# Kernel tuning notes

Measured on AMD Instinct MI355X. Metric: run time of the kernel, lower is better.

## Reference

```python
import jax, jax.numpy as jnp
import numpy as np

B, T, H, V = 32, 256, 1024, 256


def setup_inputs() -> dict:
    key = jax.random.key(0)
    ks = jax.random.split(key, 12)
    xavier = float(np.sqrt(6.0 / (H + V)))
    inp = {
        "x": jax.random.randint(ks[0], (B, T), 0, V, dtype=jnp.int64),
        "targets": jax.random.randint(ks[1], (B, T), 0, V, dtype=jnp.int64),
        "h0": jnp.zeros((B, H), jnp.float32),
        "c0": jnp.zeros((B, H), jnp.float32),
        "h1": jnp.zeros((B, H), jnp.float32),
        "c1": jnp.zeros((B, H), jnp.float32),
        # learned params
        "emb": jax.random.normal(ks[2], (V, H), jnp.float32) * 0.05,
        "W_ih0": jax.random.normal(ks[3], (H, 4 * H), jnp.float32) / np.sqrt(H),
        "W_hh0": jax.random.normal(ks[4], (H, 4 * H), jnp.float32) / np.sqrt(H),
        "b0": jnp.zeros((4 * H,), jnp.float32),
        "W_ih1": jax.random.normal(ks[5], (H, 4 * H), jnp.float32) / np.sqrt(H),
        "W_hh1": jax.random.normal(ks[6], (H, 4 * H), jnp.float32) / np.sqrt(H),
        "b1": jnp.zeros((4 * H,), jnp.float32),
        "W_out": jax.random.uniform(ks[7], (H, V), jnp.float32, -xavier, xavier),
        "b_out": jnp.zeros((V,), jnp.float32),
    }
    return inp


def _lstm_cell(h, c, inp, W_ih, W_hh, b):
    # gates: [B, 4H] -> i, f, g, o
    z = inp @ W_ih + h @ W_hh + b
    i, f, g, o = jnp.split(z, 4, axis=-1)
    c_new = jax.nn.sigmoid(f) * c + jax.nn.sigmoid(i) * jnp.tanh(g)
    h_new = jax.nn.sigmoid(o) * jnp.tanh(c_new)
    return h_new, c_new


def reference(x, targets, h0, c0, h1, c1, emb, W_ih0, W_hh0, b0,
              W_ih1, W_hh1, b1, W_out, b_out):
    # Teacher-forcing branch: embed targets, feed embedding at every step.
    embeddings = emb[targets]            # [B, T, H]
    e_seq = jnp.swapaxes(embeddings, 0, 1)  # [T, B, H] for scan over time

    def step(carry, e_t):
        (h0, c0), (h1, c1) = carry
        h0, c0 = _lstm_cell(h0, c0, e_t, W_ih0, W_hh0, b0)
        h1, c1 = _lstm_cell(h1, c1, h0, W_ih1, W_hh1, b1)
        logit = h1 @ W_out + b_out       # [B, V]
        return ((h0, c0), (h1, c1)), logit

    carry0 = ((h0, c0), (h1, c1))
    carry_f, logits_tbv = jax.lax.scan(step, carry0, e_seq)
    logits = jnp.swapaxes(logits_tbv, 0, 1)  # [B, T, V]
    (h0f, c0f), (h1f, c1f) = carry_f
    return logits, h0f, c0f, h1f, c1f
```

## Files before the change

kernel.cpp:

```cpp
#include <hip/hip_runtime.h>
#include <cstdint>


typedef float    f32x4 __attribute__((ext_vector_type(4)));
typedef short    s16x8 __attribute__((ext_vector_type(8)));
typedef unsigned u32x4 __attribute__((ext_vector_type(4)));

#define DEV __device__ __forceinline__

DEV unsigned short f2bf(float x){
  unsigned u = __builtin_bit_cast(unsigned, x);
  unsigned r = (u + 0x7fffu + ((u >> 16) & 1u)) >> 16;
  return (unsigned short)r;
}
DEV float bf2f(unsigned short b){ return __builtin_bit_cast(float, ((unsigned)b) << 16); }

DEV s16x8 ld16(const void* p){ return *(const s16x8*)p; }

DEV f32x4 MF(s16x8 a, s16x8 b, f32x4 c){
  return __builtin_amdgcn_mfma_f32_16x16x32_bf16(a, b, c, 0, 0, 0);
}

#define LDC(dst, ptr)  asm volatile("global_load_dwordx4 %0, %1, off sc0 sc1" : "=v"(dst) : "v"(ptr))
#define LDP(dst, ptr)  asm volatile("global_load_dwordx4 %0, %1, off"         : "=v"(dst) : "v"(ptr))
#define WAITVM(n) do { asm volatile("s_waitcnt vmcnt(" #n ")" ::: "memory"); \
                       __builtin_amdgcn_sched_barrier(0); } while (0)
#define CFENCE()  asm volatile("" ::: "memory")
#define TRIPLE(Cmn, Ahm, Alm, Bhn, Bln) do { \
    Cmn = MF(Ahm, Bhn, Cmn); Cmn = MF(Ahm, Bln, Cmn); Cmn = MF(Alm, Bhn, Cmn); } while (0)

DEV void st16c(void* p, u32x4 v){
  asm volatile("global_store_dwordx4 %0, %1, off sc0 sc1" :: "v"(p), "v"(v) : "memory");
}
DEV void set_flag(int* p, int v){
  __hip_atomic_store(p, v, __ATOMIC_RELAXED, __HIP_MEMORY_SCOPE_AGENT);
}
template<int SLP>
DEV void pollT(const int* f, int lane, int target){
  const int* p0 = f + lane * 8;
  const int* p1 = f + (64 + lane) * 8;
  for (;;) {
    int a = __hip_atomic_load(p0, __ATOMIC_RELAXED, __HIP_MEMORY_SCOPE_AGENT);
    int b = __hip_atomic_load(p1, __ATOMIC_RELAXED, __HIP_MEMORY_SCOPE_AGENT);
    if (__all((a >= target) && (b >= target))) break;
    __builtin_amdgcn_s_sleep(SLP);
  }
  CFENCE();
}
DEV char* h0slot(char* wa0, char* s0, char* hi, int s){
  return (s == 0) ? s0 : ((s <= 128) ? wa0 + ((size_t)(s - 1) << 17)
                                     : hi  + ((size_t)(s - 129) << 17));
}

DEV void halfgemm8(const char* smemMat, const char* ALb, const char* Bb,
                   int wgl, int ksb, int lane, f32x4 (&C)[2][2]) {
  s16x8 P[3][4], AL[3][2];
  #pragma unroll
  for (int d = 0; d < 2; ++d) {
    #pragma unroll
    for (int q = 0; q < 4; ++q) LDP(P[d][q], Bb + ((q * 32 + ksb + d) << 10) + lane * 16);
    LDP(AL[d][0], ALb + ((((wgl * 2 + 0) * 2 + 1) * 32 + ksb + d) << 10) + lane * 16);
    LDP(AL[d][1], ALb + ((((wgl * 2 + 1) * 2 + 1) * 32 + ksb + d) << 10) + lane * 16);
  }
  #pragma unroll
  for (int i = 0; i < 8; ++i) {
    const int ks = ksb + i;
    if (i < 6) {
      #pragma unroll
      for (int q = 0; q < 4; ++q) LDP(P[(i + 2) % 3][q], Bb + ((q * 32 + ks + 2) << 10) + lane * 16);
      LDP(AL[(i + 2) % 3][0], ALb + ((((wgl * 2 + 0) * 2 + 1) * 32 + ks + 2) << 10) + lane * 16);
      LDP(AL[(i + 2) % 3][1], ALb + ((((wgl * 2 + 1) * 2 + 1) * 32 + ks + 2) << 10) + lane * 16);
    }
    s16x8 Ah0 = ld16(smemMat + ((0 * 32 + ks) << 10) + lane * 16);
    s16x8 Ah1 = ld16(smemMat + ((1 * 32 + ks) << 10) + lane * 16);
    if (i < 6) { WAITVM(12); } else if (i == 6) { WAITVM(6); } else { WAITVM(0); }
    TRIPLE(C[0][0], Ah0, AL[i % 3][0], P[i % 3][0], P[i % 3][2]);
    TRIPLE(C[0][1], Ah0, AL[i % 3][0], P[i % 3][1], P[i % 3][3]);
    TRIPLE(C[1][0], Ah1, AL[i % 3][1], P[i % 3][0], P[i % 3][2]);
    TRIPLE(C[1][1], Ah1, AL[i % 3][1], P[i % 3][1], P[i % 3][3]);
  }
}

__global__ void prep_wfrag(const float* __restrict__ W0, const float* __restrict__ W1,
                           const float* __restrict__ W2, const float* __restrict__ W3,
                           char* D0, char* D1, char* D2, char* D3) {
  int gid = blockIdx.x * 256 + threadIdx.x;
  int lane = gid & 63, ks = (gid >> 6) & 31, jb = (gid >> 11) & 255, mat = gid >> 19;
  const float* S = (mat == 0) ? W0 : (mat == 1) ? W1 : (mat == 2) ? W2 : W3;
  char* D = (mat == 0) ? D0 : (mat == 1) ? D1 : (mat == 2) ? D2 : D3;
  int jp = jb * 16 + (lane & 15), u = jp >> 2, g = jp & 3;
  int kb = ks * 32 + (lane >> 4) * 8;
  s16x8 vh, vl;
  #pragma unroll
  for (int i = 0; i < 8; ++i) {
    float x = S[(kb + i) * 4096 + g * 1024 + u];
    unsigned short h = f2bf(x);
    vh[i] = (short)h;
    vl[i] = (short)f2bf(x - bf2f(h));
  }
  *(s16x8*)(D + (((jb * 2 + 0) * 32 + ks) << 10) + lane * 16) = vh;
  *(s16x8*)(D + (((jb * 2 + 1) * 32 + ks) << 10) + lane * 16) = vl;
}

__global__ void prep_bfrag(const float* __restrict__ emb, const float* __restrict__ Wout,
                           char* Demb, char* Dwout) {
  int gid = blockIdx.x * 256 + threadIdx.x;
  int lane = gid & 63, ks = (gid >> 6) & 31, vb = (gid >> 11) & 15, which = gid >> 15;
  int v = vb * 16 + (lane & 15), kb = ks * 32 + (lane >> 4) * 8;
  s16x8 vh, vl;
  #pragma unroll
  for (int i = 0; i < 8; ++i) {
    float x = which ? Wout[(kb + i) * 256 + v] : emb[v * 1024 + kb + i];
    unsigned short h = f2bf(x);
    vh[i] = (short)h;
    vl[i] = (short)f2bf(x - bf2f(h));
  }
  char* D = which ? Dwout : Demb;
  *(s16x8*)(D + (((vb * 2 + 0) * 32 + ks) << 10) + lane * 16) = vh;
  *(s16x8*)(D + (((vb * 2 + 1) * 32 + ks) << 10) + lane * 16) = vl;
}

__global__ void prep_hinit(const float* __restrict__ h0, const float* __restrict__ h1,
                           char* h0s0, char* h1f) {
  int gid = blockIdx.x * 256 + threadIdx.x;
  int lane = gid & 63, ks = (gid >> 6) & 31, nt = (gid >> 11) & 1, which = gid >> 12;
  const float* S = which ? h1 : h0;
  char* D = which ? h1f : h0s0;
  int b = nt * 16 + (lane & 15), kb = ks * 32 + (lane >> 4) * 8;
  s16x8 vh, vl;
  #pragma unroll
  for (int i = 0; i < 8; ++i) {
    float x = S[b * 1024 + kb + i];
    unsigned short h = f2bf(x);
    vh[i] = (short)h;
    vl[i] = (short)f2bf(x - bf2f(h));
  }
  *(s16x8*)(D + (((0 * 2 + nt) * 32 + ks) << 10) + lane * 16) = vh;
  *(s16x8*)(D + (((1 * 2 + nt) * 32 + ks) << 10) + lane * 16) = vl;
}

__global__ void prep_misc(const float* __restrict__ b1, float* b1i, int* f0a, int* f1a) {
  int i = blockIdx.x * 256 + threadIdx.x;
  if (i < 4096) b1i[i] = b1[(i & 3) * 1024 + (i >> 2)];
  if (i < 1024) { f0a[i] = -1; f1a[i] = -1; }
}

__global__ __launch_bounds__(256, 1) void lstm_persist(
    const int* __restrict__ tgt,
    const float* __restrict__ c0_in, const float* __restrict__ c1_in,
    const float* __restrict__ b0, const float* __restrict__ b_out,
    char* __restrict__ WA0, const char* __restrict__ WA1, const char* __restrict__ WA2,
    const char* __restrict__ WAi0, const char* __restrict__ WoutB, const char* __restrict__ embB,
    float* __restrict__ E0, const float* __restrict__ b1i,
    char* __restrict__ h0s0, char* __restrict__ h0hi, char* __restrict__ h1frag,
    int* __restrict__ f0, int* __restrict__ f1,
    float* __restrict__ out)
{
  extern __shared__ char smem[];
  constexpr int PART = 131072;
  constexpr int RP   = 131072 + 16384;
  const int tid = threadIdx.x, lane = tid & 63, wv = tid >> 6;
  const int wg = blockIdx.x;
  const bool isL0 = (wg < 128);
  const int wgl = isL0 ? wg : (wg - 128);
  const int l15 = lane & 15, l4 = lane >> 4;
  const int mi_e = wv >> 1, nt_e = wv & 1;

  __builtin_amdgcn_fence(__ATOMIC_ACQUIRE, "agent");

  if (isL0) {
    u32x4 tmp[8];
    for (int blk = 0; blk < 4; ++blk) {
      #pragma unroll
      for (int q = 0; q < 8; ++q) {
        int idx = tid + (blk * 8 + q) * 256;
        int l16 = idx & 63, ks = (idx >> 6) & 31, mi = (idx >> 11) & 1, part = idx >> 12;
        LDC(tmp[q], WA0 + ((((wgl * 2 + mi) * 2 + part) * 32 + ks) << 10) + l16 * 16);
      }
      WAITVM(0);
      #pragma unroll
      for (int q = 0; q < 8; ++q) {
        int idx = tid + (blk * 8 + q) * 256;
        int l16 = idx & 63, ks = (idx >> 6) & 31, mi = (idx >> 11) & 1, part = idx >> 12;
        *(u32x4*)(smem + (((part * 2 + mi) * 32 + ks) << 10) + l16 * 16) = tmp[q];
      }
    }
  } else {
    for (int idx = tid; idx < 8192; idx += 256) {
      int l16 = idx & 63, ks = (idx >> 6) & 31, mi = (idx >> 11) & 1, mat = idx >> 12;
      const char* W = mat ? WA2 : WA1;
      u32x4 v = *(const u32x4*)(W + ((((wgl * 2 + mi) * 2 + 0) * 32 + ks) << 10) + l16 * 16);
      *(u32x4*)(smem + (((mat * 2 + mi) * 32 + ks) << 10) + l16 * 16) = v;
    }
  }

  if (isL0) {
    f32x4 C[2][4];
    #pragma unroll
    for (int a = 0; a < 2; ++a)
      #pragma unroll
      for (int b = 0; b < 4; ++b) C[a][b] = 0.0f;
    for (int ks = 0; ks < 32; ++ks) {
      s16x8 Ah0, Ah1, Al0, Al1;
      LDC(Ah0, WAi0 + ((((wgl * 2 + 0) * 2 + 0) * 32 + ks) << 10) + lane * 16);
      LDC(Ah1, WAi0 + ((((wgl * 2 + 1) * 2 + 0) * 32 + ks) << 10) + lane * 16);
      LDC(Al0, WAi0 + ((((wgl * 2 + 0) * 2 + 1) * 32 + ks) << 10) + lane * 16);
      LDC(Al1, WAi0 + ((((wgl * 2 + 1) * 2 + 1) * 32 + ks) << 10) + lane * 16);
      WAITVM(0);
      #pragma unroll
      for (int v4 = 0; v4 < 4; ++v4) {
        int vb = wv * 4 + v4;
        s16x8 Bh = ld16(embB + (((vb * 2 + 0) * 32 + ks) << 10) + lane * 16);
        s16x8 Bl = ld16(embB + (((vb * 2 + 1) * 32 + ks) << 10) + lane * 16);
        TRIPLE(C[0][v4], Ah0, Al0, Bh, Bl);
        TRIPLE(C[1][v4], Ah1, Al1, Bh, Bl);
      }
    }
    #pragma unroll
    for (int mi = 0; mi < 2; ++mi) {
      int jb4 = wgl * 32 + mi * 16 + l4 * 4;
      int u = jb4 >> 2;
      f32x4 bb;
      #pragma unroll
      for (int r = 0; r < 4; ++r) bb[r] = b0[r * 1024 + u];
      #pragma unroll
      for (int v4 = 0; v4 < 4; ++v4) {
        int v = (wv * 4 + v4) * 16 + l15;
        *(f32x4*)(E0 + v * 4096 + jb4) = C[mi][v4] + bb;
      }
    }
  }

  float cst;
  {
    const float* cs = isL0 ? c0_in : c1_in;
    cst = cs[(nt_e * 16 + l15) * 1024 + wgl * 8 + mi_e * 4 + l4];
  }
  f32x4 b1z = {0.f, 0.f, 0.f, 0.f};
  if (!isL0) b1z = *(const f32x4*)(b1i + wgl * 32 + mi_e * 16 + (l4 << 2));

  __syncthreads();
  if (tid == 0) set_flag((isL0 ? f0 : f1) + wgl * 8, 0);

  if (isL0) {
    for (int t = 0; t < 256; ++t) {
      const int s = t + 1;
      f32x4 C[2][2];
      #pragma unroll
      for (int a = 0; a < 2; ++a)
        #pragma unroll
        for (int b = 0; b < 2; ++b) C[a][b] = 0.0f;

      int tv = tgt[(nt_e * 16 + l15) * 256 + t];
      f32x4 e0v = *(const f32x4*)(E0 + (size_t)tv * 4096 + wgl * 32 + mi_e * 16 + (l4 << 2));
      pollT<1>(f0, lane, t);
      const char* Bb = h0slot(WA0, h0s0, h0hi, t);
      const int ksb = wv * 8;
      s16x8 P[3][4];
      #pragma unroll
      for (int d = 0; d < 2; ++d)
        #pragma unroll
        for (int q = 0; q < 4; ++q) LDP(P[d][q], Bb + ((q * 32 + ksb + d) << 10) + lane * 16);
      #pragma unroll
      for (int i = 0; i < 8; ++i) {
        const int ks = ksb + i;
        if (i < 6) {
          #pragma unroll
          for (int q = 0; q < 4; ++q) LDP(P[(i + 2) % 3][q], Bb + ((q * 32 + ks + 2) << 10) + lane * 16);
        }
        s16x8 Ah0 = ld16(smem + ((0 * 32 + ks) << 10) + lane * 16);
        s16x8 Ah1 = ld16(smem + ((1 * 32 + ks) << 10) + lane * 16);
        s16x8 Al0 = ld16(smem + ((2 * 32 + ks) << 10) + lane * 16);
        s16x8 Al1 = ld16(smem + ((3 * 32 + ks) << 10) + lane * 16);
        if (i < 6) { WAITVM(8); } else if (i == 6) { WAITVM(4); } else { WAITVM(0); }
        TRIPLE(C[0][0], Ah0, Al0, P[i % 3][0], P[i % 3][2]);
        TRIPLE(C[0][1], Ah0, Al0, P[i % 3][1], P[i % 3][3]);
        TRIPLE(C[1][0], Ah1, Al1, P[i % 3][0], P[i % 3][2]);
        TRIPLE(C[1][1], Ah1, Al1, P[i % 3][1], P[i % 3][3]);
      }

      #pragma unroll
      for (int mi = 0; mi < 2; ++mi)
        #pragma unroll
        for (int nt = 0; nt < 2; ++nt)
          *(f32x4*)(smem + PART + ((wv * 4 + mi * 2 + nt) << 10) + lane * 16) = C[mi][nt];
      __syncthreads();

      {
        f32x4 z = *(const f32x4*)(smem + PART + ((0 * 4 + wv) << 10) + lane * 16);
        #pragma unroll
        for (int w = 1; w < 4; ++w)
          z += *(const f32x4*)(smem + PART + ((w * 4 + wv) << 10) + lane * 16);
        z += e0v;
        float ig = 1.f / (1.f + __expf(-z[0]));
        float fg = 1.f / (1.f + __expf(-z[1]));
        float og = 1.f / (1.f + __expf(-z[3]));
        float cn = fg * cst + ig * tanhf(z[2]);
        float hn = og * tanhf(cn);
        cst = cn;
        unsigned short hb = f2bf(hn);
        unsigned short lb = f2bf(hn - bf2f(hb));
        *(short*)(smem + RP + ((0 + nt_e) * 16 + l15) * 16 + (mi_e * 4 + l4) * 2) = (short)hb;
        *(short*)(smem + RP + ((2 + nt_e) * 16 + l15) * 16 + (mi_e * 4 + l4) * 2) = (short)lb;
        if (t == 255) {
          int u = wgl * 8 + mi_e * 4 + l4, b = nt_e * 16 + l15;
          out[2097152 + b * 1024 + u] = hn;
          out[2097152 + 32768 + b * 1024 + u] = cn;
        }
      }
      __syncthreads();

      if (wv == 0) {
        char* hd = h0slot(WA0, h0s0, h0hi, s);
        u32x4 v = *(const u32x4*)(smem + RP + lane * 16);
        char* dst = hd + (((lane >> 4) * 32 + (wgl >> 2)) << 10) + ((wgl & 3) * 16 + l15) * 16;
        st16c(dst, v);
        asm volatile("s_waitcnt vmcnt(0)" ::: "memory");
        if (lane == 0) set_flag(f0 + wgl * 8, s);
      }
    }
  } else {
    f32x4 zpre;
    {
      pollT<2>(f0, lane, 1);
      f32x4 C2[2][2];
      #pragma unroll
      for (int a = 0; a < 2; ++a)
        #pragma unroll
        for (int b = 0; b < 2; ++b) C2[a][b] = 0.0f;
      halfgemm8(smem, WA1, h0slot(WA0, h0s0, h0hi, 1), wgl, wv * 8, lane, C2);
      #pragma unroll
      for (int mi = 0; mi < 2; ++mi)
        #pragma unroll
        for (int nt = 0; nt < 2; ++nt)
          *(f32x4*)(smem + PART + ((wv * 4 + mi * 2 + nt) << 10) + lane * 16) = C2[mi][nt];
      __syncthreads();
      zpre = *(const f32x4*)(smem + PART + ((0 * 4 + wv) << 10) + lane * 16);
      #pragma unroll
      for (int w = 1; w < 4; ++w)
        zpre += *(const f32x4*)(smem + PART + ((w * 4 + wv) << 10) + lane * 16);
      __syncthreads();
    }

    for (int t = 0; t < 256; ++t) {
      const int s = t + 1;
      f32x4 C[2][2];
      #pragma unroll
      for (int a = 0; a < 2; ++a)
        #pragma unroll
        for (int b = 0; b < 2; ++b) C[a][b] = 0.0f;

      pollT<1>(f1, lane, t);
      halfgemm8(smem + 65536, WA2, h1frag + (size_t)t * 131072, wgl, wv * 8, lane, C);

      #pragma unroll
      for (int mi = 0; mi < 2; ++mi)
        #pragma unroll
        for (int nt = 0; nt < 2; ++nt)
          *(f32x4*)(smem + PART + ((wv * 4 + mi * 2 + nt) << 10) + lane * 16) = C[mi][nt];
      __syncthreads();

      {
        f32x4 z = *(const f32x4*)(smem + PART + ((0 * 4 + wv) << 10) + lane * 16);
        #pragma unroll
        for (int w = 1; w < 4; ++w)
          z += *(const f32x4*)(smem + PART + ((w * 4 + wv) << 10) + lane * 16);
        z += zpre + b1z;
        float ig = 1.f / (1.f + __expf(-z[0]));
        float fg = 1.f / (1.f + __expf(-z[1]));
        float og = 1.f / (1.f + __expf(-z[3]));
        float cn = fg * cst + ig * tanhf(z[2]);
        float hn = og * tanhf(cn);
        cst = cn;
        unsigned short hb = f2bf(hn);
        unsigned short lb = f2bf(hn - bf2f(hb));
        *(short*)(smem + RP + ((0 + nt_e) * 16 + l15) * 16 + (mi_e * 4 + l4) * 2) = (short)hb;
        *(short*)(smem + RP + ((2 + nt_e) * 16 + l15) * 16 + (mi_e * 4 + l4) * 2) = (short)lb;
        if (t == 255) {
          int u = wgl * 8 + mi_e * 4 + l4, b = nt_e * 16 + l15;
          out[2097152 + 65536 + b * 1024 + u] = hn;
          out[2097152 + 65536 + 32768 + b * 1024 + u] = cn;
        }
      }
      __syncthreads();

      if (wv == 0) {
        char* hd = h1frag + (size_t)s * 131072;
        u32x4 v = *(const u32x4*)(smem + RP + lane * 16);
        char* dst = hd + (((lane >> 4) * 32 + (wgl >> 2)) << 10) + ((wgl & 3) * 16 + l15) * 16;
        st16c(dst, v);
        asm volatile("s_waitcnt vmcnt(0)" ::: "memory");
        if (lane == 0) set_flag(f1 + wgl * 8, s);
      }

      if (t < 255) {
        pollT<2>(f0, lane, t + 2);
        f32x4 C2[2][2];
        #pragma unroll
        for (int a = 0; a < 2; ++a)
          #pragma unroll
          for (int b = 0; b < 2; ++b) C2[a][b] = 0.0f;
        halfgemm8(smem, WA1, h0slot(WA0, h0s0, h0hi, t + 2), wgl, wv * 8, lane, C2);
        #pragma unroll
        for (int mi = 0; mi < 2; ++mi)
          #pragma unroll
          for (int nt = 0; nt < 2; ++nt)
            *(f32x4*)(smem + PART + ((wv * 4 + mi * 2 + nt) << 10) + lane * 16) = C2[mi][nt];
        __syncthreads();
        zpre = *(const f32x4*)(smem + PART + ((0 * 4 + wv) << 10) + lane * 16);
        #pragma unroll
        for (int w = 1; w < 4; ++w)
          zpre += *(const f32x4*)(smem + PART + ((w * 4 + wv) << 10) + lane * 16);
        __syncthreads();
      }
    }
  }

  {
    const int tp = isL0 ? wgl : (128 + wgl);
    pollT<32>(f1, lane, tp + 1);
    const char* A = h1frag + (size_t)(tp + 1) * 131072;
    f32x4 C[2][4];
    #pragma unroll
    for (int a = 0; a < 2; ++a)
      #pragma unroll
      for (int b = 0; b < 4; ++b) C[a][b] = 0.0f;
    s16x8 QA[4], QB[4];
    #pragma unroll
    for (int q = 0; q < 4; ++q) LDP(QA[q], A + ((q * 32 + 0) << 10) + lane * 16);
    for (int kk = 0; kk < 16; ++kk) {
      const int ks = kk * 2;
      #pragma unroll
      for (int q = 0; q < 4; ++q) LDP(QB[q], A + ((q * 32 + ks + 1) << 10) + lane * 16);
      asm volatile("s_waitcnt vmcnt(4)" ::: "memory");
      __builtin_amdgcn_sched_barrier(0);
      #pragma unroll
      for (int v4 = 0; v4 < 4; ++v4) {
        int vb = wv * 4 + v4;
        s16x8 Bh = ld16(WoutB + (((vb * 2 + 0) * 32 + ks) << 10) + lane * 16);
        s16x8 Bl = ld16(WoutB + (((vb * 2 + 1) * 32 + ks) << 10) + lane * 16);
        C[0][v4] = MF(QA[0], Bh, C[0][v4]); C[0][v4] = MF(QA[0], Bl, C[0][v4]); C[0][v4] = MF(QA[2], Bh, C[0][v4]);
        C[1][v4] = MF(QA[1], Bh, C[1][v4]); C[1][v4] = MF(QA[1], Bl, C[1][v4]); C[1][v4] = MF(QA[3], Bh, C[1][v4]);
      }
      if (kk < 15) {
        #pragma unroll
        for (int q = 0; q < 4; ++q) LDP(QA[q], A + ((q * 32 + ks + 2) << 10) + lane * 16);
        asm volatile("s_waitcnt vmcnt(4)" ::: "memory");
      } else {
        asm volatile("s_waitcnt vmcnt(0)" ::: "memory");
      }
      __builtin_amdgcn_sched_barrier(0);
      #pragma unroll
      for (int v4 = 0; v4 < 4; ++v4) {
        int vb = wv * 4 + v4;
        s16x8 Bh = ld16(WoutB + (((vb * 2 + 0) * 32 + ks + 1) << 10) + lane * 16);
        s16x8 Bl = ld16(WoutB + (((vb * 2 + 1) * 32 + ks + 1) << 10) + lane * 16);
        C[0][v4] = MF(QB[0], Bh, C[0][v4]); C[0][v4] = MF(QB[0], Bl, C[0][v4]); C[0][v4] = MF(QB[2], Bh, C[0][v4]);
        C[1][v4] = MF(QB[1], Bh, C[1][v4]); C[1][v4] = MF(QB[1], Bl, C[1][v4]); C[1][v4] = MF(QB[3], Bh, C[1][v4]);
      }
    }
    #pragma unroll
    for (int nt = 0; nt < 2; ++nt)
      #pragma unroll
      for (int v4 = 0; v4 < 4; ++v4) {
        int v = (wv * 4 + v4) * 16 + l15;
        float bo = b_out[v];
        #pragma unroll
        for (int r = 0; r < 4; ++r) {
          int b = nt * 16 + l4 * 4 + r;
          out[((size_t)b * 256 + tp) * 256 + v] = C[nt][v4][r] + bo;
        }
      }
  }
}

extern "C" void kernel_launch(void* const* d_in, const int* in_sizes, int n_in,
                              void* d_out, int out_size, void* d_ws, size_t ws_size,
                              hipStream_t stream) {
  const int*   targets = (const int*)d_in[1];
  const float* h0_in   = (const float*)d_in[2];
  const float* c0_in   = (const float*)d_in[3];
  const float* h1_in   = (const float*)d_in[4];
  const float* c1_in   = (const float*)d_in[5];
  const float* emb     = (const float*)d_in[6];
  const float* W_ih0   = (const float*)d_in[7];
  const float* W_hh0   = (const float*)d_in[8];
  const float* b0      = (const float*)d_in[9];
  const float* W_ih1   = (const float*)d_in[10];
  const float* W_hh1   = (const float*)d_in[11];
  const float* b1      = (const float*)d_in[12];
  const float* W_out   = (const float*)d_in[13];
  const float* b_out   = (const float*)d_in[14];
  float* out = (float*)d_out;

  char* ws = (char*)d_ws;
  char*  WA0    = ws;
  char*  WA1    = ws + 16777216;
  char*  WA2    = ws + 33554432;
  char*  WoutB  = ws + 50331648;
  char*  embB   = ws + 51380224;
  float* E0     = (float*)(ws + 52428800);
  float* b1i    = (float*)(ws + 56623104);
  int*   f0     = (int*)(ws + 56639488);
  int*   f1     = (int*)(ws + 56643584);
  char*  h0s0   = ws + 56647680;
  char*  h0hi   = ws + 56778752;
  char*  h1frag = ws + 73555968;
  char*  WAi0   = h1frag + 16777216;

  prep_misc <<<18,   256, 0, stream>>>(b1, b1i, f0, f1);
  prep_wfrag<<<8192, 256, 0, stream>>>(W_hh0, W_ih1, W_hh1, W_ih0, WA0, WA1, WA2, WAi0);
  prep_bfrag<<<256,  256, 0, stream>>>(emb, W_out, embB, WoutB);
  prep_hinit<<<32,   256, 0, stream>>>(h0_in, h1_in, h0s0, h1frag);

  hipFuncSetAttribute(reinterpret_cast<const void*>(lstm_persist),
                      hipFuncAttributeMaxDynamicSharedMemorySize, 148480);
  lstm_persist<<<256, 256, 148480, stream>>>(
      targets, c0_in, c1_in, b0, b_out,
      WA0, WA1, WA2, WAi0, WoutB, embB,
      E0, b1i, h0s0, h0hi, h1frag, f0, f1, out);
}
```

Baseline: 1.729 ms.

## Split layer-1 waves between recurrent and input GEMMs and pack flags

In layer-1 workgroups, two waves now compute the recurrent W_hh1·h1 half-GEMM over 16 k-steps while the other two compute the next step's W_ih1·h0 input projection. The input projection is double-buffered in shared memory, which removes the serial second GEMM phase and its two extra barriers from each timestep. Progress flags are also packed contiguously instead of spaced 8 ints apart, so each poll touches fewer cache lines. The recurrent critical path now runs on half the waves with longer k-loops, and shared memory use grows.

```diff
diff --git a/kernel.cpp b/kernel.cpp
--- a/kernel.cpp
+++ b/kernel.cpp
@@ -36,9 +36,9 @@
   __hip_atomic_store(p, v, __ATOMIC_RELAXED, __HIP_MEMORY_SCOPE_AGENT);
 }
 template<int SLP>
-DEV void pollT(const int* f, int lane, int target){
-  const int* p0 = f + lane * 8;
-  const int* p1 = f + (64 + lane) * 8;
+DEV void pollP(const int* f, int lane, int target){
+  const int* p0 = f + lane;
+  const int* p1 = f + 64 + lane;
   for (;;) {
     int a = __hip_atomic_load(p0, __ATOMIC_RELAXED, __HIP_MEMORY_SCOPE_AGENT);
     int b = __hip_atomic_load(p1, __ATOMIC_RELAXED, __HIP_MEMORY_SCOPE_AGENT);
@@ -52,7 +52,8 @@
                                      : hi  + ((size_t)(s - 129) << 17));
 }
 
-DEV void halfgemm8(const char* smemMat, const char* ALb, const char* Bb,
+template<int ITERS>
+DEV void halfgemmT(const char* smemMat, const char* ALb, const char* Bb,
                    int wgl, int ksb, int lane, f32x4 (&C)[2][2]) {
   s16x8 P[3][4], AL[3][2];
   #pragma unroll
@@ -63,9 +64,9 @@
     LDP(AL[d][1], ALb + ((((wgl * 2 + 1) * 2 + 1) * 32 + ksb + d) << 10) + lane * 16);
   }
   #pragma unroll
-  for (int i = 0; i < 8; ++i) {
+  for (int i = 0; i < ITERS; ++i) {
     const int ks = ksb + i;
-    if (i < 6) {
+    if (i < ITERS - 2) {
       #pragma unroll
       for (int q = 0; q < 4; ++q) LDP(P[(i + 2) % 3][q], Bb + ((q * 32 + ks + 2) << 10) + lane * 16);
       LDP(AL[(i + 2) % 3][0], ALb + ((((wgl * 2 + 0) * 2 + 1) * 32 + ks + 2) << 10) + lane * 16);
@@ -73,7 +74,7 @@
     }
     s16x8 Ah0 = ld16(smemMat + ((0 * 32 + ks) << 10) + lane * 16);
     s16x8 Ah1 = ld16(smemMat + ((1 * 32 + ks) << 10) + lane * 16);
-    if (i < 6) { WAITVM(12); } else if (i == 6) { WAITVM(6); } else { WAITVM(0); }
+    if (i < ITERS - 2) { WAITVM(12); } else if (i == ITERS - 2) { WAITVM(6); } else { WAITVM(0); }
     TRIPLE(C[0][0], Ah0, AL[i % 3][0], P[i % 3][0], P[i % 3][2]);
     TRIPLE(C[0][1], Ah0, AL[i % 3][0], P[i % 3][1], P[i % 3][3]);
     TRIPLE(C[1][0], Ah1, AL[i % 3][1], P[i % 3][0], P[i % 3][2]);
@@ -157,8 +158,11 @@
     float* __restrict__ out)
 {
   extern __shared__ char smem[];
-  constexpr int PART = 131072;
-  constexpr int RP   = 131072 + 16384;
+  constexpr int PART  = 131072;
+  constexpr int RP0   = 131072 + 16384;
+  constexpr int PARTc = 131072;
+  constexpr int ZPRE  = 131072 + 8192;
+  constexpr int RP1   = 131072 + 24576;
   const int tid = threadIdx.x, lane = tid & 63, wv = tid >> 6;
   const int wg = blockIdx.x;
   const bool isL0 = (wg < 128);
@@ -240,7 +244,7 @@
   if (!isL0) b1z = *(const f32x4*)(b1i + wgl * 32 + mi_e * 16 + (l4 << 2));
 
   __syncthreads();
-  if (tid == 0) set_flag((isL0 ? f0 : f1) + wgl * 8, 0);
+  if (tid == 0) set_flag((isL0 ? f0 : f1) + wgl, 0);
 
   if (isL0) {
     for (int t = 0; t < 256; ++t) {
@@ -253,7 +257,7 @@
 
       int tv = tgt[(nt_e * 16 + l15) * 256 + t];
       f32x4 e0v = *(const f32x4*)(E0 + (size_t)tv * 4096 + wgl * 32 + mi_e * 16 + (l4 << 2));
-      pollT<1>(f0, lane, t);
+      pollP<1>(f0, lane, t);
       const char* Bb = h0slot(WA0, h0s0, h0hi, t);
       const int ksb = wv * 8;
       s16x8 P[3][4];
@@ -300,8 +304,8 @@
         cst = cn;
         unsigned short hb = f2bf(hn);
         unsigned short lb = f2bf(hn - bf2f(hb));
-        *(short*)(smem + RP + ((0 + nt_e) * 16 + l15) * 16 + (mi_e * 4 + l4) * 2) = (short)hb;
-        *(short*)(smem + RP + ((2 + nt_e) * 16 + l15) * 16 + (mi_e * 4 + l4) * 2) = (short)lb;
+        *(short*)(smem + RP0 + ((0 + nt_e) * 16 + l15) * 16 + (mi_e * 4 + l4) * 2) = (short)hb;
+        *(short*)(smem + RP0 + ((2 + nt_e) * 16 + l15) * 16 + (mi_e * 4 + l4) * 2) = (short)lb;
         if (t == 255) {
           int u = wgl * 8 + mi_e * 4 + l4, b = nt_e * 16 + l15;
           out[2097152 + b * 1024 + u] = hn;
@@ -312,60 +316,69 @@
 
       if (wv == 0) {
         char* hd = h0slot(WA0, h0s0, h0hi, s);
-        u32x4 v = *(const u32x4*)(smem + RP + lane * 16);
+        u32x4 v = *(const u32x4*)(smem + RP0 + lane * 16);
         char* dst = hd + (((lane >> 4) * 32 + (wgl >> 2)) << 10) + ((wgl & 3) * 16 + l15) * 16;
         st16c(dst, v);
         asm volatile("s_waitcnt vmcnt(0)" ::: "memory");
-        if (lane == 0) set_flag(f0 + wgl * 8, s);
+        if (lane == 0) set_flag(f0 + wgl, s);
       }
     }
   } else {
-    f32x4 zpre;
-    {
-      pollT<2>(f0, lane, 1);
-      f32x4 C2[2][2];
+    pollP<2>(f0, lane, 1);
+    if (wv >= 2) {
+      f32x4 C[2][2];
       #pragma unroll
       for (int a = 0; a < 2; ++a)
         #pragma unroll
-        for (int b = 0; b < 2; ++b) C2[a][b] = 0.0f;
-      halfgemm8(smem, WA1, h0slot(WA0, h0s0, h0hi, 1), wgl, wv * 8, lane, C2);
+        for (int b = 0; b < 2; ++b) C[a][b] = 0.0f;
+      halfgemmT<16>(smem, WA1, h0slot(WA0, h0s0, h0hi, 1), wgl, (wv - 2) * 16, lane, C);
       #pragma unroll
       for (int mi = 0; mi < 2; ++mi)
         #pragma unroll
         for (int nt = 0; nt < 2; ++nt)
-          *(f32x4*)(smem + PART + ((wv * 4 + mi * 2 + nt) << 10) + lane * 16) = C2[mi][nt];
-      __syncthreads();
-      zpre = *(const f32x4*)(smem + PART + ((0 * 4 + wv) << 10) + lane * 16);
-      #pragma unroll
-      for (int w = 1; w < 4; ++w)
-        zpre += *(const f32x4*)(smem + PART + ((w * 4 + wv) << 10) + lane * 16);
-      __syncthreads();
+          *(f32x4*)(smem + ZPRE + ((0 * 8 + (wv - 2) * 4 + mi * 2 + nt) << 10) + lane * 16) = C[mi][nt];
     }
 
     for (int t = 0; t < 256; ++t) {
       const int s = t + 1;
-      f32x4 C[2][2];
-      #pragma unroll
-      for (int a = 0; a < 2; ++a)
-        #pragma unroll
-        for (int b = 0; b < 2; ++b) C[a][b] = 0.0f;
-
-      pollT<1>(f1, lane, t);
-      halfgemm8(smem + 65536, WA2, h1frag + (size_t)t * 131072, wgl, wv * 8, lane, C);
-
-      #pragma unroll
-      for (int mi = 0; mi < 2; ++mi)
-        #pragma unroll
-        for (int nt = 0; nt < 2; ++nt)
-          *(f32x4*)(smem + PART + ((wv * 4 + mi * 2 + nt) << 10) + lane * 16) = C[mi][nt];
+      const int cur = t & 1;
+      pollP<1>(f1, lane, t);
+      if (t < 255) pollP<2>(f0, lane, t + 2);
+
+      if (wv < 2) {
+        f32x4 C[2][2];
+        #pragma unroll
+        for (int a = 0; a < 2; ++a)
+          #pragma unroll
+          for (int b = 0; b < 2; ++b) C[a][b] = 0.0f;
+        halfgemmT<16>(smem + 65536, WA2, h1frag + (size_t)t * 131072, wgl, wv * 16, lane, C);
+        #pragma unroll
+        for (int mi = 0; mi < 2; ++mi)
+          #pragma unroll
+          for (int nt = 0; nt < 2; ++nt)
+            *(f32x4*)(smem + PARTc + ((wv * 4 + mi * 2 + nt) << 10) + lane * 16) = C[mi][nt];
+      } else {
+        f32x4 C[2][2];
+        #pragma unroll
+        for (int a = 0; a < 2; ++a)
+          #pragma unroll
+          for (int b = 0; b < 2; ++b) C[a][b] = 0.0f;
+        const int sl = (t < 255) ? (t + 2) : 256;
+        halfgemmT<16>(smem, WA1, h0slot(WA0, h0s0, h0hi, sl), wgl, (wv - 2) * 16, lane, C);
+        #pragma unroll
+        for (int mi = 0; mi < 2; ++mi)
+          #pragma unroll
+          for (int nt = 0; nt < 2; ++nt)
+            *(f32x4*)(smem + ZPRE + (((cur ^ 1) * 8 + (wv - 2) * 4 + mi * 2 + nt) << 10) + lane * 16) = C[mi][nt];
+      }
       __syncthreads();
 
       {
-        f32x4 z = *(const f32x4*)(smem + PART + ((0 * 4 + wv) << 10) + lane * 16);
-        #pragma unroll
-        for (int w = 1; w < 4; ++w)
-          z += *(const f32x4*)(smem + PART + ((w * 4 + wv) << 10) + lane * 16);
-        z += zpre + b1z;
+        f32x4 z = *(const f32x4*)(smem + PARTc + ((0 * 4 + wv) << 10) + lane * 16);
+        z += *(const f32x4*)(smem + PARTc + ((1 * 4 + wv) << 10) + lane * 16);
+        z += *(const f32x4*)(smem + ZPRE + ((cur * 8 + 0 * 4 + wv) << 10) + lane * 16);
+        z += *(const f32x4*)(smem + ZPRE + ((cur * 8 + 1 * 4 + wv) << 10) + lane * 16);
+        z += b1z;
         float ig = 1.f / (1.f + __expf(-z[0]));
         float fg = 1.f / (1.f + __expf(-z[1]));
         float og = 1.f / (1.f + __expf(-z[3]));
@@ -374,8 +387,8 @@
         cst = cn;
         unsigned short hb = f2bf(hn);
         unsigned short lb = f2bf(hn - bf2f(hb));
-        *(short*)(smem + RP + ((0 + nt_e) * 16 + l15) * 16 + (mi_e * 4 + l4) * 2) = (short)hb;
-        *(short*)(smem + RP + ((2 + nt_e) * 16 + l15) * 16 + (mi_e * 4 + l4) * 2) = (short)lb;
+        *(short*)(smem + RP1 + ((0 + nt_e) * 16 + l15) * 16 + (mi_e * 4 + l4) * 2) = (short)hb;
+        *(short*)(smem + RP1 + ((2 + nt_e) * 16 + l15) * 16 + (mi_e * 4 + l4) * 2) = (short)lb;
         if (t == 255) {
           int u = wgl * 8 + mi_e * 4 + l4, b = nt_e * 16 + l15;
           out[2097152 + 65536 + b * 1024 + u] = hn;
@@ -386,39 +399,18 @@
 
       if (wv == 0) {
         char* hd = h1frag + (size_t)s * 131072;
-        u32x4 v = *(const u32x4*)(smem + RP + lane * 16);
+        u32x4 v = *(const u32x4*)(smem + RP1 + lane * 16);
         char* dst = hd + (((lane >> 4) * 32 + (wgl >> 2)) << 10) + ((wgl & 3) * 16 + l15) * 16;
         st16c(dst, v);
         asm volatile("s_waitcnt vmcnt(0)" ::: "memory");
-        if (lane == 0) set_flag(f1 + wgl * 8, s);
-      }
-
-      if (t < 255) {
-        pollT<2>(f0, lane, t + 2);
-        f32x4 C2[2][2];
-        #pragma unroll
-        for (int a = 0; a < 2; ++a)
-          #pragma unroll
-          for (int b = 0; b < 2; ++b) C2[a][b] = 0.0f;
-        halfgemm8(smem, WA1, h0slot(WA0, h0s0, h0hi, t + 2), wgl, wv * 8, lane, C2);
-        #pragma unroll
-        for (int mi = 0; mi < 2; ++mi)
-          #pragma unroll
-          for (int nt = 0; nt < 2; ++nt)
-            *(f32x4*)(smem + PART + ((wv * 4 + mi * 2 + nt) << 10) + lane * 16) = C2[mi][nt];
-        __syncthreads();
-        zpre = *(const f32x4*)(smem + PART + ((0 * 4 + wv) << 10) + lane * 16);
-        #pragma unroll
-        for (int w = 1; w < 4; ++w)
-          zpre += *(const f32x4*)(smem + PART + ((w * 4 + wv) << 10) + lane * 16);
-        __syncthreads();
+        if (lane == 0) set_flag(f1 + wgl, s);
       }
     }
   }
 
   {
     const int tp = isL0 ? wgl : (128 + wgl);
-    pollT<32>(f1, lane, tp + 1);
+    pollP<32>(f1, lane, tp + 1);
     const char* A = h1frag + (size_t)(tp + 1) * 131072;
     f32x4 C[2][4];
     #pragma unroll
@@ -514,8 +506,8 @@
   prep_hinit<<<32,   256, 0, stream>>>(h0_in, h1_in, h0s0, h1frag);
 
   hipFuncSetAttribute(reinterpret_cast<const void*>(lstm_persist),
-                      hipFuncAttributeMaxDynamicSharedMemorySize, 148480);
-  lstm_persist<<<256, 256, 148480, stream>>>(
+                      hipFuncAttributeMaxDynamicSharedMemorySize, 156672);
+  lstm_persist<<<256, 256, 156672, stream>>>(
       targets, c0_in, c1_in, b0, b_out,
       WA0, WA1, WA2, WAi0, WoutB, embB,
       E0, b1i, h0s0, h0hi, h1frag, f0, f1, out);
```

Result: slower. 3.233 ms (+87.0%).

## Issue all K-slab loads up front and pack sync flags contiguously

Applied to the files above, without the earlier changes.

Replaces the 3-deep rotating prefetch in the recurrent GEMMs with issuing all eight K-step loads at once, then draining them with descending vmcnt waits. This puts more memory requests in flight right after each flag poll, to hide global latency on the serial time-step critical path. It also packs the per-workgroup progress flags densely instead of spacing them 32 bytes apart, so each poll touches fewer cache lines. The cost is much higher VGPR use from holding 8x4 (plus 8x2) fragments, which risks spills. Densely packed flags also put several workgroups' flag writes on the same line.

```diff
diff --git a/kernel.cpp b/kernel.cpp
--- a/kernel.cpp
+++ b/kernel.cpp
@@ -29,6 +29,11 @@
 #define TRIPLE(Cmn, Ahm, Alm, Bhn, Bln) do { \
     Cmn = MF(Ahm, Bhn, Cmn); Cmn = MF(Ahm, Bln, Cmn); Cmn = MF(Alm, Bhn, Cmn); } while (0)
 
+template<int N> DEV void waitvm(){
+  __builtin_amdgcn_s_waitcnt((N & 15) | (7 << 4) | (15 << 8) | ((N >> 4) << 14));
+  __builtin_amdgcn_sched_barrier(0);
+}
+
 DEV void st16c(void* p, u32x4 v){
   asm volatile("global_store_dwordx4 %0, %1, off sc0 sc1" :: "v"(p), "v"(v) : "memory");
 }
@@ -36,9 +41,9 @@
   __hip_atomic_store(p, v, __ATOMIC_RELAXED, __HIP_MEMORY_SCOPE_AGENT);
 }
 template<int SLP>
-DEV void pollT(const int* f, int lane, int target){
-  const int* p0 = f + lane * 8;
-  const int* p1 = f + (64 + lane) * 8;
+DEV void pollP(const int* f, int lane, int target){
+  const int* p0 = f + lane;
+  const int* p1 = f + 64 + lane;
   for (;;) {
     int a = __hip_atomic_load(p0, __ATOMIC_RELAXED, __HIP_MEMORY_SCOPE_AGENT);
     int b = __hip_atomic_load(p1, __ATOMIC_RELAXED, __HIP_MEMORY_SCOPE_AGENT);
@@ -52,33 +57,27 @@
                                      : hi  + ((size_t)(s - 129) << 17));
 }
 
-DEV void halfgemm8(const char* smemMat, const char* ALb, const char* Bb,
-                   int wgl, int ksb, int lane, f32x4 (&C)[2][2]) {
-  s16x8 P[3][4], AL[3][2];
+DEV void gemm6(const char* smemMat, const char* ALb, const char* Bb,
+               int wgl, int ksb, int lane, f32x4 (&C)[2][2]) {
+  s16x8 P[8][4], AL[8][2];
   #pragma unroll
-  for (int d = 0; d < 2; ++d) {
+  for (int d = 0; d < 8; ++d) {
     #pragma unroll
     for (int q = 0; q < 4; ++q) LDP(P[d][q], Bb + ((q * 32 + ksb + d) << 10) + lane * 16);
     LDP(AL[d][0], ALb + ((((wgl * 2 + 0) * 2 + 1) * 32 + ksb + d) << 10) + lane * 16);
     LDP(AL[d][1], ALb + ((((wgl * 2 + 1) * 2 + 1) * 32 + ksb + d) << 10) + lane * 16);
   }
-  #pragma unroll
-  for (int i = 0; i < 8; ++i) {
-    const int ks = ksb + i;
-    if (i < 6) {
-      #pragma unroll
-      for (int q = 0; q < 4; ++q) LDP(P[(i + 2) % 3][q], Bb + ((q * 32 + ks + 2) << 10) + lane * 16);
-      LDP(AL[(i + 2) % 3][0], ALb + ((((wgl * 2 + 0) * 2 + 1) * 32 + ks + 2) << 10) + lane * 16);
-      LDP(AL[(i + 2) % 3][1], ALb + ((((wgl * 2 + 1) * 2 + 1) * 32 + ks + 2) << 10) + lane * 16);
-    }
-    s16x8 Ah0 = ld16(smemMat + ((0 * 32 + ks) << 10) + lane * 16);
-    s16x8 Ah1 = ld16(smemMat + ((1 * 32 + ks) << 10) + lane * 16);
-    if (i < 6) { WAITVM(12); } else if (i == 6) { WAITVM(6); } else { WAITVM(0); }
-    TRIPLE(C[0][0], Ah0, AL[i % 3][0], P[i % 3][0], P[i % 3][2]);
-    TRIPLE(C[0][1], Ah0, AL[i % 3][0], P[i % 3][1], P[i % 3][3]);
-    TRIPLE(C[1][0], Ah1, AL[i % 3][1], P[i % 3][0], P[i % 3][2]);
-    TRIPLE(C[1][1], Ah1, AL[i % 3][1], P[i % 3][1], P[i % 3][3]);
-  }
+#define G6IT(i, W) { const int ks = ksb + i; \
+    s16x8 Ah0 = ld16(smemMat + ((0 * 32 + ks) << 10) + lane * 16); \
+    s16x8 Ah1 = ld16(smemMat + ((1 * 32 + ks) << 10) + lane * 16); \
+    waitvm<W>(); \
+    TRIPLE(C[0][0], Ah0, AL[i][0], P[i][0], P[i][2]); \
+    TRIPLE(C[0][1], Ah0, AL[i][0], P[i][1], P[i][3]); \
+    TRIPLE(C[1][0], Ah1, AL[i][1], P[i][0], P[i][2]); \
+    TRIPLE(C[1][1], Ah1, AL[i][1], P[i][1], P[i][3]); }
+  G6IT(0, 42) G6IT(1, 36) G6IT(2, 30) G6IT(3, 24)
+  G6IT(4, 18) G6IT(5, 12) G6IT(6, 6)  G6IT(7, 0)
+#undef G6IT
 }
 
 __global__ void prep_wfrag(const float* __restrict__ W0, const float* __restrict__ W1,
@@ -240,7 +239,7 @@
   if (!isL0) b1z = *(const f32x4*)(b1i + wgl * 32 + mi_e * 16 + (l4 << 2));
 
   __syncthreads();
-  if (tid == 0) set_flag((isL0 ? f0 : f1) + wgl * 8, 0);
+  if (tid == 0) set_flag((isL0 ? f0 : f1) + wgl, 0);
 
   if (isL0) {
     for (int t = 0; t < 256; ++t) {
@@ -253,31 +252,27 @@
 
       int tv = tgt[(nt_e * 16 + l15) * 256 + t];
       f32x4 e0v = *(const f32x4*)(E0 + (size_t)tv * 4096 + wgl * 32 + mi_e * 16 + (l4 << 2));
-      pollT<1>(f0, lane, t);
+      pollP<1>(f0, lane, t);
       const char* Bb = h0slot(WA0, h0s0, h0hi, t);
       const int ksb = wv * 8;
-      s16x8 P[3][4];
-      #pragma unroll
-      for (int d = 0; d < 2; ++d)
+      s16x8 P[8][4];
+      #pragma unroll
+      for (int d = 0; d < 8; ++d)
         #pragma unroll
         for (int q = 0; q < 4; ++q) LDP(P[d][q], Bb + ((q * 32 + ksb + d) << 10) + lane * 16);
-      #pragma unroll
-      for (int i = 0; i < 8; ++i) {
-        const int ks = ksb + i;
-        if (i < 6) {
-          #pragma unroll
-          for (int q = 0; q < 4; ++q) LDP(P[(i + 2) % 3][q], Bb + ((q * 32 + ks + 2) << 10) + lane * 16);
-        }
-        s16x8 Ah0 = ld16(smem + ((0 * 32 + ks) << 10) + lane * 16);
-        s16x8 Ah1 = ld16(smem + ((1 * 32 + ks) << 10) + lane * 16);
-        s16x8 Al0 = ld16(smem + ((2 * 32 + ks) << 10) + lane * 16);
-        s16x8 Al1 = ld16(smem + ((3 * 32 + ks) << 10) + lane * 16);
-        if (i < 6) { WAITVM(8); } else if (i == 6) { WAITVM(4); } else { WAITVM(0); }
-        TRIPLE(C[0][0], Ah0, Al0, P[i % 3][0], P[i % 3][2]);
-        TRIPLE(C[0][1], Ah0, Al0, P[i % 3][1], P[i % 3][3]);
-        TRIPLE(C[1][0], Ah1, Al1, P[i % 3][0], P[i % 3][2]);
-        TRIPLE(C[1][1], Ah1, Al1, P[i % 3][1], P[i % 3][3]);
-      }
+#define L0IT(i, W) { const int ks = ksb + i; \
+      s16x8 Ah0 = ld16(smem + ((0 * 32 + ks) << 10) + lane * 16); \
+      s16x8 Ah1 = ld16(smem + ((1 * 32 + ks) << 10) + lane * 16); \
+      s16x8 Al0 = ld16(smem + ((2 * 32 + ks) << 10) + lane * 16); \
+      s16x8 Al1 = ld16(smem + ((3 * 32 + ks) << 10) + lane * 16); \
+      waitvm<W>(); \
+      TRIPLE(C[0][0], Ah0, Al0, P[i][0], P[i][2]); \
+      TRIPLE(C[0][1], Ah0, Al0, P[i][1], P[i][3]); \
+      TRIPLE(C[1][0], Ah1, Al1, P[i][0], P[i][2]); \
+      TRIPLE(C[1][1], Ah1, Al1, P[i][1], P[i][3]); }
+      L0IT(0, 28) L0IT(1, 24) L0IT(2, 20) L0IT(3, 16)
+      L0IT(4, 12) L0IT(5, 8)  L0IT(6, 4)  L0IT(7, 0)
+#undef L0IT
 
       #pragma unroll
       for (int mi = 0; mi < 2; ++mi)
@@ -316,19 +311,19 @@
         char* dst = hd + (((lane >> 4) * 32 + (wgl >> 2)) << 10) + ((wgl & 3) * 16 + l15) * 16;
         st16c(dst, v);
         asm volatile("s_waitcnt vmcnt(0)" ::: "memory");
-        if (lane == 0) set_flag(f0 + wgl * 8, s);
+        if (lane == 0) set_flag(f0 + wgl, s);
       }
     }
   } else {
     f32x4 zpre;
     {
-      pollT<2>(f0, lane, 1);
+      pollP<2>(f0, lane, 1);
       f32x4 C2[2][2];
       #pragma unroll
       for (int a = 0; a < 2; ++a)
         #pragma unroll
         for (int b = 0; b < 2; ++b) C2[a][b] = 0.0f;
-      halfgemm8(smem, WA1, h0slot(WA0, h0s0, h0hi, 1), wgl, wv * 8, lane, C2);
+      gemm6(smem, WA1, h0slot(WA0, h0s0, h0hi, 1), wgl, wv * 8, lane, C2);
       #pragma unroll
       for (int mi = 0; mi < 2; ++mi)
         #pragma unroll
@@ -350,8 +345,8 @@
         #pragma unroll
         for (int b = 0; b < 2; ++b) C[a][b] = 0.0f;
 
-      pollT<1>(f1, lane, t);
-      halfgemm8(smem + 65536, WA2, h1frag + (size_t)t * 131072, wgl, wv * 8, lane, C);
+      pollP<1>(f1, lane, t);
+      gemm6(smem + 65536, WA2, h1frag + (size_t)t * 131072, wgl, wv * 8, lane, C);
 
       #pragma unroll
       for (int mi = 0; mi < 2; ++mi)
@@ -390,17 +385,17 @@
         char* dst = hd + (((lane >> 4) * 32 + (wgl >> 2)) << 10) + ((wgl & 3) * 16 + l15) * 16;
         st16c(dst, v);
         asm volatile("s_waitcnt vmcnt(0)" ::: "memory");
-        if (lane == 0) set_flag(f1 + wgl * 8, s);
+        if (lane == 0) set_flag(f1 + wgl, s);
       }
 
       if (t < 255) {
-        pollT<2>(f0, lane, t + 2);
+        pollP<2>(f0, lane, t + 2);
         f32x4 C2[2][2];
         #pragma unroll
         for (int a = 0; a < 2; ++a)
           #pragma unroll
           for (int b = 0; b < 2; ++b) C2[a][b] = 0.0f;
-        halfgemm8(smem, WA1, h0slot(WA0, h0s0, h0hi, t + 2), wgl, wv * 8, lane, C2);
+        gemm6(smem, WA1, h0slot(WA0, h0s0, h0hi, t + 2), wgl, wv * 8, lane, C2);
         #pragma unroll
         for (int mi = 0; mi < 2; ++mi)
           #pragma unroll
@@ -418,7 +413,7 @@
 
   {
     const int tp = isL0 ? wgl : (128 + wgl);
-    pollT<32>(f1, lane, tp + 1);
+    pollP<32>(f1, lane, tp + 1);
     const char* A = h1frag + (size_t)(tp + 1) * 131072;
     f32x4 C[2][4];
     #pragma unroll
```

New measurement: 2.607 ms. 50.8% more time.
